# Optimization experiments

Measured on AMD Instinct MI355X. Metric: run time of the kernel, lower is better.

Reference implementation:

```python
import jax, jax.numpy as jnp
import numpy as np

EPS = 1e-10


def setup_inputs() -> dict:
    key = jax.random.key(0)
    k1, k2 = jax.random.split(key)
    x = jax.random.normal(k1, (64, 512, 256), dtype=jnp.float32)          # (N, code_dim, T)
    codebooks = jax.random.normal(k2, (6, 1024, 512), dtype=jnp.float32)  # (Q, nb_code, code_dim)
    return {"x": x, "codebooks": codebooks}


def _quantize_layer(x_flat, cb):
    # x_flat: (NT, D), cb: (C, D)
    dist = (jnp.sum(x_flat * x_flat, axis=-1, keepdims=True)
            - 2.0 * (x_flat @ cb.T)
            + jnp.sum(cb * cb, axis=-1))          # (NT, C)
    idx = jnp.argmin(dist, axis=-1)               # (NT,)
    x_d = cb[idx]                                 # gather, (NT, D)
    return idx, x_d


def reference(x, codebooks):
    N, D, T = x.shape
    Q, C, _ = codebooks.shape
    NT = N * T

    residual = x
    quantized_out = jnp.zeros_like(x)
    all_indices, losses, perps = [], [], []

    for q in range(Q):  # fixed small number of sequential quantizer stages
        cb = codebooks[q]
        # preprocess: (N, D, T) -> (NT, D)
        x_flat = residual.transpose(0, 2, 1).reshape(NT, D)
        idx, x_d = _quantize_layer(x_flat, cb)

        # commitment loss (codebook side detached; EMA-trained codebook)
        commit_loss = jnp.mean((x_flat - jax.lax.stop_gradient(x_d)) ** 2)

        # perplexity of code usage
        probs = jnp.zeros((C,), dtype=x.dtype).at[idx].add(1.0) / NT
        perplexity = jnp.exp(-jnp.sum(probs * jnp.log(probs + EPS)))

        # straight-through estimator, back to (N, D, T)
        quantized = x_flat + jax.lax.stop_gradient(x_d - x_flat)
        quantized = quantized.reshape(N, T, D).transpose(0, 2, 1)

        residual = residual - jax.lax.stop_gradient(quantized)
        quantized_out = quantized_out + quantized

        all_indices.append(idx.reshape(N, T))
        losses.append(commit_loss)
        perps.append(perplexity)

    all_indices = jnp.stack(all_indices, axis=-1)      # (N, T, Q)
    mean_loss = sum(losses) / Q
    mean_perplexity = sum(perps) / Q
    return quantized_out, all_indices, mean_loss, mean_perplexity
```

## Files before the change

### kernel.cpp

```cpp
#include <hip/hip_runtime.h>
#include <hip/hip_fp16.h>
#include <hip/hip_bf16.h>
#include <stdint.h>


#define NTROWS 16384
#define DDIM   512
#define CCODES 1024
#define QSTAGE 6

#define OFF_R      ((size_t)0)
#define OFF_RBF    ((size_t)33554432)
#define OFF_CBBF   ((size_t)50331648)
#define OFF_CAND   ((size_t)56623104)
#define OFF_CBSQ   ((size_t)58720256)
#define OFF_HIST   ((size_t)58744832)
#define OFF_LOSS   ((size_t)58769408)
#define WS_END     ((size_t)58775552)

#define OUT_IDX_OFF  ((size_t)8388608)
#define OUT_SCAL_OFF ((size_t)8486912)

typedef __attribute__((ext_vector_type(8))) short short8;
typedef __attribute__((ext_vector_type(8))) unsigned short ushort8v;
typedef __attribute__((ext_vector_type(4))) float f32x4;

__device__ __forceinline__ unsigned short f2bf(float f) {
    uint32_t u = __float_as_uint(f);
    uint32_t r = (u + 0x7fffu + ((u >> 16) & 1u)) >> 16;
    return (unsigned short)r;
}
__device__ __forceinline__ uint32_t fkey(float f) {
    uint32_t u = __float_as_uint(f);
    return u ^ ((uint32_t)((int32_t)u >> 31) | 0x80000000u);
}
__device__ __forceinline__ float funkey(uint32_t k) {
    uint32_t u = (k & 0x80000000u) ? (k ^ 0x80000000u) : ~k;
    return __uint_as_float(u);
}
__device__ __forceinline__ uint32_t umin32(uint32_t a, uint32_t b) { return a < b ? a : b; }
__device__ __forceinline__ uint32_t umax32(uint32_t a, uint32_t b) { return a > b ? a : b; }
__device__ __forceinline__ float wave_sum(float v) {
    for (int m = 32; m; m >>= 1) v += __shfl_xor(v, m, 64);
    return v;
}
__device__ __forceinline__ uint32_t wave_min_u32(uint32_t v) {
    for (int m = 32; m; m >>= 1) v = umin32(v, (uint32_t)__shfl_xor((int)v, m, 64));
    return v;
}
__device__ __forceinline__ void async_load16(const void* g, void* l) {
    __builtin_amdgcn_global_load_lds(
        (__attribute__((address_space(1))) void*)(void*)g,
        (__attribute__((address_space(3))) void*)l, 16, 0, 0);
}

__global__ __launch_bounds__(256) void prep_kernel(
    const float* __restrict__ x, const float* __restrict__ cb,
    float* __restrict__ r, unsigned short* __restrict__ rbf,
    unsigned short* __restrict__ cbbf, float* __restrict__ cbsq,
    unsigned int* __restrict__ hist, float* __restrict__ loss_bins)
{
    __shared__ float tile[32][33];
    if (blockIdx.x < 1536) {
        const int wave = threadIdx.x >> 6, lane = threadIdx.x & 63;
        const int row = blockIdx.x * 4 + wave;
        const float* p = cb + (size_t)row * DDIM;
        unsigned short* pb = cbbf + (size_t)row * DDIM;
        float s = 0.f;
#pragma unroll
        for (int t = 0; t < 8; ++t) {
            float v = p[lane + 64 * t];
            pb[lane + 64 * t] = f2bf(v);
            s += v * v;
        }
        s = wave_sum(s);
        if (lane == 0) cbsq[row] = s;
        if (blockIdx.x == 0) {
            for (int i = threadIdx.x; i < QSTAGE * CCODES; i += 256) hist[i] = 0u;
            for (int i = threadIdx.x; i < QSTAGE * 256; i += 256) loss_bins[i] = 0.f;
        }
    } else {
        const int bidx = blockIdx.x - 1536;
        const int d0 = (bidx & 15) * 32;
        const int t0 = ((bidx >> 4) & 7) * 32;
        const int n  = bidx >> 7;
        const int tx = threadIdx.x & 31, ty = threadIdx.x >> 5;
        const float* xp = x + (size_t)n * (DDIM * 256);
#pragma unroll
        for (int s = 0; s < 4; ++s) {
            int dd = ty + s * 8;
            tile[dd][tx] = xp[(size_t)(d0 + dd) * 256 + t0 + tx];
        }
        __syncthreads();
#pragma unroll
        for (int s = 0; s < 4; ++s) {
            int tt = ty + s * 8;
            float v = tile[tx][tt];
            size_t off = (size_t)(n * 256 + t0 + tt) * DDIM + d0 + tx;
            r[off] = v;
            rbf[off] = f2bf(v);
        }
    }
}

__global__ __launch_bounds__(256, 2) void gemm_dist_kernel(
    const unsigned short* __restrict__ Abf,
    const unsigned short* __restrict__ Bbf,
    const float* __restrict__ cbsq,
    uint32_t* __restrict__ cand)
{
    __shared__ __align__(16) unsigned short lA[128 * 32];
    __shared__ __align__(16) unsigned short lB[256 * 32];
    const int tid = threadIdx.x;
    const int wave = tid >> 6, lane = tid & 63;
    const int quad = lane >> 4, l15 = lane & 15;
    const int tm = blockIdx.x, tn2 = blockIdx.y;
    const int wm = wave & 1, wn = wave >> 1;

    f32x4 acc[4][8];
#pragma unroll
    for (int i = 0; i < 4; ++i)
#pragma unroll
        for (int j = 0; j < 8; ++j) acc[i][j] = (f32x4){0.f, 0.f, 0.f, 0.f};

    const int srow = wave * 16 + (lane >> 2);
    const int gchunk = (lane & 3) ^ ((lane >> 3) & 3);
    const unsigned short* gA0 = Abf + (size_t)(tm * 128 + srow) * DDIM + gchunk * 8;
    const unsigned short* gA1 = gA0 + 64 * DDIM;
    const unsigned short* gB0 = Bbf + (size_t)(tn2 * 256 + srow) * DDIM + gchunk * 8;
    const unsigned short* gB1 = gB0 + 64 * DDIM;
    const unsigned short* gB2 = gB0 + 128 * DDIM;
    const unsigned short* gB3 = gB0 + 192 * DDIM;
    unsigned short* sA0 = &lA[srow * 32 + (lane & 3) * 8];
    unsigned short* sA1 = &lA[(64 + srow) * 32 + (lane & 3) * 8];
    unsigned short* sB0 = &lB[srow * 32 + (lane & 3) * 8];
    unsigned short* sB1 = &lB[(64 + srow) * 32 + (lane & 3) * 8];
    unsigned short* sB2 = &lB[(128 + srow) * 32 + (lane & 3) * 8];
    unsigned short* sB3 = &lB[(192 + srow) * 32 + (lane & 3) * 8];

    for (int kt = 0; kt < DDIM / 32; ++kt) {
        async_load16(gA0, sA0); async_load16(gA1, sA1);
        async_load16(gB0, sB0); async_load16(gB1, sB1);
        async_load16(gB2, sB2); async_load16(gB3, sB3);
        gA0 += 32; gA1 += 32; gB0 += 32; gB1 += 32; gB2 += 32; gB3 += 32;
        __syncthreads();
        const int cqa = (quad ^ ((l15 >> 1) & 3)) * 8;
        short8 af[4], bfr[8];
#pragma unroll
        for (int i = 0; i < 4; ++i)
            af[i] = *(const short8*)&lA[(wm * 64 + i * 16 + l15) * 32 + cqa];
#pragma unroll
        for (int j = 0; j < 8; ++j)
            bfr[j] = *(const short8*)&lB[(wn * 128 + j * 16 + l15) * 32 + cqa];
#pragma unroll
        for (int i = 0; i < 4; ++i)
#pragma unroll
            for (int j = 0; j < 8; ++j)
                acc[i][j] = __builtin_amdgcn_mfma_f32_16x16x32_bf16(
                    af[i], bfr[j], acc[i][j], 0, 0, 0);
        __syncthreads();
    }

    const int rowbase = tm * 128 + wm * 64 + quad * 4;
    const int colbase = tn2 * 256 + wn * 128 + l15;
    const int gbase = tn2 * 4 + wn * 2;
    float cbs[8];
#pragma unroll
    for (int j = 0; j < 8; ++j) cbs[j] = cbsq[colbase + j * 16];
#pragma unroll
    for (int i = 0; i < 4; ++i) {
#pragma unroll
        for (int reg = 0; reg < 4; ++reg) {
            const int row = rowbase + i * 16 + reg;
#pragma unroll
            for (int jh = 0; jh < 2; ++jh) {
                uint32_t k[4];
#pragma unroll
                for (int jj = 0; jj < 4; ++jj) {
                    const int j = jh * 4 + jj;
                    float dv = cbs[j] - 2.0f * acc[i][j][reg];
                    k[jj] = (fkey(dv) & ~1023u) | (uint32_t)(colbase + j * 16);
                }
                uint32_t m01 = umin32(k[0], k[1]), M01 = umax32(k[0], k[1]);
                uint32_t m23 = umin32(k[2], k[3]), M23 = umax32(k[2], k[3]);
                uint32_t k1 = umin32(m01, m23);
                uint32_t k2 = umin32(umax32(m01, m23), umin32(M01, M23));
#pragma unroll
                for (int m = 1; m < 16; m <<= 1) {
                    uint32_t o1 = (uint32_t)__shfl_xor((int)k1, m, 64);
                    uint32_t o2 = (uint32_t)__shfl_xor((int)k2, m, 64);
                    uint32_t n1 = umin32(k1, o1);
                    uint32_t n2 = umin32(umax32(k1, o1), umin32(k2, o2));
                    k1 = n1; k2 = n2;
                }
                if (l15 == 0)
                    *(uint2*)&cand[((size_t)row * 16 + gbase + jh) * 2] =
                        make_uint2(k1, k2);
            }
        }
    }
}

#define MARGIN 8.0f
__global__ __launch_bounds__(256) void refine_kernel(
    float* __restrict__ r, unsigned short* __restrict__ rbf,
    const float* __restrict__ cbq, const float* __restrict__ cbsqq,
    const uint32_t* __restrict__ cand,
    float* __restrict__ out_idx, unsigned int* __restrict__ histq,
    float* __restrict__ loss_bins, int q, int write_bf)
{
    const int wave = threadIdx.x >> 6, lane = threadIdx.x & 63;
    const int nt = blockIdx.x * 4 + wave;

    const float4* r4 = (const float4*)(r + (size_t)nt * DDIM);
    float4 ra = r4[lane * 2], rb = r4[lane * 2 + 1];
    float s = ra.x * ra.x + ra.y * ra.y + ra.z * ra.z + ra.w * ra.w
            + rb.x * rb.x + rb.y * rb.y + rb.z * rb.z + rb.w * rb.w;
    const float sumx = wave_sum(s);

    uint32_t key = 0xFFFFFFFFu;
    if (lane < 32) key = cand[(size_t)nt * 32 + lane];
    const uint32_t kmin = wave_min_u32(key);
    const float thr = funkey(kmin & ~1023u) + MARGIN;

    unsigned long long mask = __ballot(lane < 32 && funkey(key & ~1023u) <= thr);

    float best = 1e30f;
    int bestc = CCODES;
    while (mask) {
        const int src = __ffsll(mask) - 1;
        mask &= mask - 1;
        const int cc = __shfl((int)(key & 1023u), src, 64);
        const float4* crow = (const float4*)(cbq + (size_t)cc * DDIM);
        float4 ca = crow[lane * 2], cb2 = crow[lane * 2 + 1];
        float dot = ra.x * ca.x + ra.y * ca.y + ra.z * ca.z + ra.w * ca.w
                  + rb.x * cb2.x + rb.y * cb2.y + rb.z * cb2.z + rb.w * cb2.w;
        dot = wave_sum(dot);
        const float de = (sumx - 2.0f * dot) + cbsqq[cc];
        if (de < best || (de == best && cc < bestc)) { best = de; bestc = cc; }
    }

    const float4* cbest = (const float4*)(cbq + (size_t)bestc * DDIM);
    float4 ba = cbest[lane * 2], bb = cbest[lane * 2 + 1];
    float4 na = make_float4(ra.x - ba.x, ra.y - ba.y, ra.z - ba.z, ra.w - ba.w);
    float4 nb = make_float4(rb.x - bb.x, rb.y - bb.y, rb.z - bb.z, rb.w - bb.w);
    float4* rw = (float4*)(r + (size_t)nt * DDIM);
    rw[lane * 2] = na; rw[lane * 2 + 1] = nb;
    if (write_bf) {
        ushort8v pk;
        pk[0] = f2bf(na.x); pk[1] = f2bf(na.y); pk[2] = f2bf(na.z); pk[3] = f2bf(na.w);
        pk[4] = f2bf(nb.x); pk[5] = f2bf(nb.y); pk[6] = f2bf(nb.z); pk[7] = f2bf(nb.w);
        *(ushort8v*)(rbf + (size_t)nt * DDIM + lane * 8) = pk;
    }

    if (lane == 0) {
        out_idx[(size_t)nt * QSTAGE + q] = (float)bestc;
        atomicAdd(&histq[bestc], 1u);
        atomicAdd(&loss_bins[q * 256 + (blockIdx.x & 255)], best);
    }
}

__global__ __launch_bounds__(256) void final_kernel(
    const float* __restrict__ x, const float* __restrict__ r,
    float* __restrict__ out,
    const unsigned int* __restrict__ hist, const float* __restrict__ loss_bins,
    float* __restrict__ out2)
{
    __shared__ float tile[32][33];
    __shared__ float red[4];
    __shared__ float perp_acc;
    const int tid = threadIdx.x, wave = tid >> 6, lane = tid & 63;

    if (blockIdx.x < 8192) {
        const int bidx = blockIdx.x;
        const int d0 = (bidx & 15) * 32;
        const int t0 = ((bidx >> 4) & 7) * 32;
        const int n  = bidx >> 7;
        const int tx = tid & 31, ty = tid >> 5;
#pragma unroll
        for (int s = 0; s < 4; ++s) {
            int tt = ty + s * 8;
            tile[tt][tx] = r[(size_t)(n * 256 + t0 + tt) * DDIM + d0 + tx];
        }
        __syncthreads();
        const float* xp = x + (size_t)n * (DDIM * 256);
        float* op = out + (size_t)n * (DDIM * 256);
#pragma unroll
        for (int s = 0; s < 4; ++s) {
            int dd = ty + s * 8;
            size_t off = (size_t)(d0 + dd) * 256 + t0 + tx;
            op[off] = xp[off] - tile[tx][dd];
        }
        return;
    }

    if (tid == 0) perp_acc = 0.f;
    __syncthreads();
    for (int q = 0; q < QSTAGE; ++q) {
        float s = 0.f;
        for (int c = tid; c < CCODES; c += 256) {
            float p = (float)hist[q * CCODES + c] * (1.0f / (float)NTROWS);
            s += p * logf(p + 1e-10f);
        }
        s = wave_sum(s);
        if (lane == 0) red[wave] = s;
        __syncthreads();
        if (tid == 0) {
            float tot = red[0] + red[1] + red[2] + red[3];
            perp_acc += expf(-tot);
        }
        __syncthreads();
    }
    float ls = 0.f;
    for (int i = tid; i < QSTAGE * 256; i += 256) ls += loss_bins[i];
    ls = wave_sum(ls);
    if (lane == 0) red[wave] = ls;
    __syncthreads();
    if (tid == 0) {
        float lsum = red[0] + red[1] + red[2] + red[3];
        out2[0] = (lsum / (float)QSTAGE) / ((float)NTROWS * (float)DDIM);
        out2[1] = perp_acc / (float)QSTAGE;
    }
}

extern "C" void kernel_launch(void* const* d_in, const int* in_sizes, int n_in,
                              void* d_out, int out_size, void* d_ws, size_t ws_size,
                              hipStream_t stream)
{
    const float* x  = (const float*)d_in[0];
    const float* cb = (const float*)d_in[1];
    float* out = (float*)d_out;
    char* ws = (char*)d_ws;

    float*          r      = (float*)(ws + OFF_R);
    unsigned short* rbf    = (unsigned short*)(ws + OFF_RBF);
    unsigned short* cbbf   = (unsigned short*)(ws + OFF_CBBF);
    uint32_t*       cand   = (uint32_t*)(ws + OFF_CAND);
    float*          cbsq   = (float*)(ws + OFF_CBSQ);
    unsigned int*   hist   = (unsigned int*)(ws + OFF_HIST);
    float*          lbins  = (float*)(ws + OFF_LOSS);

    prep_kernel<<<9728, 256, 0, stream>>>(x, cb, r, rbf, cbbf, cbsq, hist, lbins);

    for (int q = 0; q < QSTAGE; ++q) {
        const size_t cboff = (size_t)q * CCODES * DDIM;
        gemm_dist_kernel<<<dim3(128, 4), 256, 0, stream>>>(
            rbf, cbbf + cboff, cbsq + q * CCODES, cand);
        refine_kernel<<<4096, 256, 0, stream>>>(
            r, rbf, cb + cboff, cbsq + q * CCODES, cand,
            out + OUT_IDX_OFF, hist + q * CCODES, lbins,
            q, (q < QSTAGE - 1) ? 1 : 0);
    }

    final_kernel<<<8193, 256, 0, stream>>>(x, r, out, hist, lbins,
                                           out + OUT_SCAL_OFF);
}
```

Before: 476.0 us.

## Fuse previous-stage refine into next-stage distance GEMM with ping-pong buffers

Each stage's exact refine step now runs at the start of the next stage's bf16 distance GEMM kernel. Each block refines its own 128 rows and writes fp32 and bf16 residuals before loading them as the GEMM A operand. Residuals and candidate lists ping-pong between two buffers, one of which is the output buffer used as scratch. The final stage keeps a standalone refine kernel. This removes one launch per stage and a residual round trip, but the refine is repeated by all four column blocks for the same rows and runs serially, 32 rows per wave, with much less parallelism. The candidate margin also tightens from 8 to 2, and the A-operand loads get a cache-policy bit.

```diff
diff --git a/kernel.cpp b/kernel.cpp
--- a/kernel.cpp
+++ b/kernel.cpp
@@ -9,17 +9,20 @@
 #define CCODES 1024
 #define QSTAGE 6
 
-#define OFF_R      ((size_t)0)
+#define OFF_R0     ((size_t)0)
 #define OFF_RBF    ((size_t)33554432)
 #define OFF_CBBF   ((size_t)50331648)
-#define OFF_CAND   ((size_t)56623104)
-#define OFF_CBSQ   ((size_t)58720256)
-#define OFF_HIST   ((size_t)58744832)
-#define OFF_LOSS   ((size_t)58769408)
-#define WS_END     ((size_t)58775552)
+#define OFF_CAND0  ((size_t)56623104)
+#define OFF_CAND1  ((size_t)58720256)
+#define OFF_CBSQ   ((size_t)60817408)
+#define OFF_HIST   ((size_t)60841984)
+#define OFF_LOSS   ((size_t)60866560)
+#define WS_END     ((size_t)60872704)
 
 #define OUT_IDX_OFF  ((size_t)8388608)
 #define OUT_SCAL_OFF ((size_t)8486912)
+
+#define MARGIN 2.0f
 
 typedef __attribute__((ext_vector_type(8))) short short8;
 typedef __attribute__((ext_vector_type(8))) unsigned short ushort8v;
@@ -48,181 +51,26 @@
     for (int m = 32; m; m >>= 1) v = umin32(v, (uint32_t)__shfl_xor((int)v, m, 64));
     return v;
 }
+template <int AUX>
 __device__ __forceinline__ void async_load16(const void* g, void* l) {
     __builtin_amdgcn_global_load_lds(
         (__attribute__((address_space(1))) void*)(void*)g,
-        (__attribute__((address_space(3))) void*)l, 16, 0, 0);
-}
-
-__global__ __launch_bounds__(256) void prep_kernel(
-    const float* __restrict__ x, const float* __restrict__ cb,
-    float* __restrict__ r, unsigned short* __restrict__ rbf,
-    unsigned short* __restrict__ cbbf, float* __restrict__ cbsq,
-    unsigned int* __restrict__ hist, float* __restrict__ loss_bins)
-{
-    __shared__ float tile[32][33];
-    if (blockIdx.x < 1536) {
-        const int wave = threadIdx.x >> 6, lane = threadIdx.x & 63;
-        const int row = blockIdx.x * 4 + wave;
-        const float* p = cb + (size_t)row * DDIM;
-        unsigned short* pb = cbbf + (size_t)row * DDIM;
-        float s = 0.f;
-#pragma unroll
-        for (int t = 0; t < 8; ++t) {
-            float v = p[lane + 64 * t];
-            pb[lane + 64 * t] = f2bf(v);
-            s += v * v;
-        }
-        s = wave_sum(s);
-        if (lane == 0) cbsq[row] = s;
-        if (blockIdx.x == 0) {
-            for (int i = threadIdx.x; i < QSTAGE * CCODES; i += 256) hist[i] = 0u;
-            for (int i = threadIdx.x; i < QSTAGE * 256; i += 256) loss_bins[i] = 0.f;
-        }
-    } else {
-        const int bidx = blockIdx.x - 1536;
-        const int d0 = (bidx & 15) * 32;
-        const int t0 = ((bidx >> 4) & 7) * 32;
-        const int n  = bidx >> 7;
-        const int tx = threadIdx.x & 31, ty = threadIdx.x >> 5;
-        const float* xp = x + (size_t)n * (DDIM * 256);
-#pragma unroll
-        for (int s = 0; s < 4; ++s) {
-            int dd = ty + s * 8;
-            tile[dd][tx] = xp[(size_t)(d0 + dd) * 256 + t0 + tx];
-        }
-        __syncthreads();
-#pragma unroll
-        for (int s = 0; s < 4; ++s) {
-            int tt = ty + s * 8;
-            float v = tile[tx][tt];
-            size_t off = (size_t)(n * 256 + t0 + tt) * DDIM + d0 + tx;
-            r[off] = v;
-            rbf[off] = f2bf(v);
-        }
-    }
-}
-
-__global__ __launch_bounds__(256, 2) void gemm_dist_kernel(
-    const unsigned short* __restrict__ Abf,
-    const unsigned short* __restrict__ Bbf,
-    const float* __restrict__ cbsq,
-    uint32_t* __restrict__ cand)
-{
-    __shared__ __align__(16) unsigned short lA[128 * 32];
-    __shared__ __align__(16) unsigned short lB[256 * 32];
-    const int tid = threadIdx.x;
-    const int wave = tid >> 6, lane = tid & 63;
-    const int quad = lane >> 4, l15 = lane & 15;
-    const int tm = blockIdx.x, tn2 = blockIdx.y;
-    const int wm = wave & 1, wn = wave >> 1;
-
-    f32x4 acc[4][8];
-#pragma unroll
-    for (int i = 0; i < 4; ++i)
-#pragma unroll
-        for (int j = 0; j < 8; ++j) acc[i][j] = (f32x4){0.f, 0.f, 0.f, 0.f};
-
-    const int srow = wave * 16 + (lane >> 2);
-    const int gchunk = (lane & 3) ^ ((lane >> 3) & 3);
-    const unsigned short* gA0 = Abf + (size_t)(tm * 128 + srow) * DDIM + gchunk * 8;
-    const unsigned short* gA1 = gA0 + 64 * DDIM;
-    const unsigned short* gB0 = Bbf + (size_t)(tn2 * 256 + srow) * DDIM + gchunk * 8;
-    const unsigned short* gB1 = gB0 + 64 * DDIM;
-    const unsigned short* gB2 = gB0 + 128 * DDIM;
-    const unsigned short* gB3 = gB0 + 192 * DDIM;
-    unsigned short* sA0 = &lA[srow * 32 + (lane & 3) * 8];
-    unsigned short* sA1 = &lA[(64 + srow) * 32 + (lane & 3) * 8];
-    unsigned short* sB0 = &lB[srow * 32 + (lane & 3) * 8];
-    unsigned short* sB1 = &lB[(64 + srow) * 32 + (lane & 3) * 8];
-    unsigned short* sB2 = &lB[(128 + srow) * 32 + (lane & 3) * 8];
-    unsigned short* sB3 = &lB[(192 + srow) * 32 + (lane & 3) * 8];
-
-    for (int kt = 0; kt < DDIM / 32; ++kt) {
-        async_load16(gA0, sA0); async_load16(gA1, sA1);
-        async_load16(gB0, sB0); async_load16(gB1, sB1);
-        async_load16(gB2, sB2); async_load16(gB3, sB3);
-        gA0 += 32; gA1 += 32; gB0 += 32; gB1 += 32; gB2 += 32; gB3 += 32;
-        __syncthreads();
-        const int cqa = (quad ^ ((l15 >> 1) & 3)) * 8;
-        short8 af[4], bfr[8];
-#pragma unroll
-        for (int i = 0; i < 4; ++i)
-            af[i] = *(const short8*)&lA[(wm * 64 + i * 16 + l15) * 32 + cqa];
-#pragma unroll
-        for (int j = 0; j < 8; ++j)
-            bfr[j] = *(const short8*)&lB[(wn * 128 + j * 16 + l15) * 32 + cqa];
-#pragma unroll
-        for (int i = 0; i < 4; ++i)
-#pragma unroll
-            for (int j = 0; j < 8; ++j)
-                acc[i][j] = __builtin_amdgcn_mfma_f32_16x16x32_bf16(
-                    af[i], bfr[j], acc[i][j], 0, 0, 0);
-        __syncthreads();
-    }
-
-    const int rowbase = tm * 128 + wm * 64 + quad * 4;
-    const int colbase = tn2 * 256 + wn * 128 + l15;
-    const int gbase = tn2 * 4 + wn * 2;
-    float cbs[8];
-#pragma unroll
-    for (int j = 0; j < 8; ++j) cbs[j] = cbsq[colbase + j * 16];
-#pragma unroll
-    for (int i = 0; i < 4; ++i) {
-#pragma unroll
-        for (int reg = 0; reg < 4; ++reg) {
-            const int row = rowbase + i * 16 + reg;
-#pragma unroll
-            for (int jh = 0; jh < 2; ++jh) {
-                uint32_t k[4];
-#pragma unroll
-                for (int jj = 0; jj < 4; ++jj) {
-                    const int j = jh * 4 + jj;
-                    float dv = cbs[j] - 2.0f * acc[i][j][reg];
-                    k[jj] = (fkey(dv) & ~1023u) | (uint32_t)(colbase + j * 16);
-                }
-                uint32_t m01 = umin32(k[0], k[1]), M01 = umax32(k[0], k[1]);
-                uint32_t m23 = umin32(k[2], k[3]), M23 = umax32(k[2], k[3]);
-                uint32_t k1 = umin32(m01, m23);
-                uint32_t k2 = umin32(umax32(m01, m23), umin32(M01, M23));
-#pragma unroll
-                for (int m = 1; m < 16; m <<= 1) {
-                    uint32_t o1 = (uint32_t)__shfl_xor((int)k1, m, 64);
-                    uint32_t o2 = (uint32_t)__shfl_xor((int)k2, m, 64);
-                    uint32_t n1 = umin32(k1, o1);
-                    uint32_t n2 = umin32(umax32(k1, o1), umin32(k2, o2));
-                    k1 = n1; k2 = n2;
-                }
-                if (l15 == 0)
-                    *(uint2*)&cand[((size_t)row * 16 + gbase + jh) * 2] =
-                        make_uint2(k1, k2);
-            }
-        }
-    }
-}
-
-#define MARGIN 8.0f
-__global__ __launch_bounds__(256) void refine_kernel(
-    float* __restrict__ r, unsigned short* __restrict__ rbf,
-    const float* __restrict__ cbq, const float* __restrict__ cbsqq,
-    const uint32_t* __restrict__ cand,
-    float* __restrict__ out_idx, unsigned int* __restrict__ histq,
-    float* __restrict__ loss_bins, int q, int write_bf)
-{
-    const int wave = threadIdx.x >> 6, lane = threadIdx.x & 63;
-    const int nt = blockIdx.x * 4 + wave;
-
-    const float4* r4 = (const float4*)(r + (size_t)nt * DDIM);
-    float4 ra = r4[lane * 2], rb = r4[lane * 2 + 1];
+        (__attribute__((address_space(3))) void*)l, 16, 0, AUX);
+}
+
+__device__ __forceinline__ void refine_core(
+    int nt, int lane, float4 ra, float4 rb, uint32_t key,
+    float* r_out, unsigned short* rbf,
+    const float* cbq, const float* cbsqq,
+    float* out_idx, unsigned int* histq, float* loss_bins,
+    int q, int write_bf, int do_side)
+{
     float s = ra.x * ra.x + ra.y * ra.y + ra.z * ra.z + ra.w * ra.w
             + rb.x * rb.x + rb.y * rb.y + rb.z * rb.z + rb.w * rb.w;
     const float sumx = wave_sum(s);
 
-    uint32_t key = 0xFFFFFFFFu;
-    if (lane < 32) key = cand[(size_t)nt * 32 + lane];
     const uint32_t kmin = wave_min_u32(key);
     const float thr = funkey(kmin & ~1023u) + MARGIN;
-
     unsigned long long mask = __ballot(lane < 32 && funkey(key & ~1023u) <= thr);
 
     float best = 1e30f;
@@ -244,7 +92,7 @@
     float4 ba = cbest[lane * 2], bb = cbest[lane * 2 + 1];
     float4 na = make_float4(ra.x - ba.x, ra.y - ba.y, ra.z - ba.z, ra.w - ba.w);
     float4 nb = make_float4(rb.x - bb.x, rb.y - bb.y, rb.z - bb.z, rb.w - bb.w);
-    float4* rw = (float4*)(r + (size_t)nt * DDIM);
+    float4* rw = (float4*)(r_out + (size_t)nt * DDIM);
     rw[lane * 2] = na; rw[lane * 2 + 1] = nb;
     if (write_bf) {
         ushort8v pk;
@@ -252,12 +100,202 @@
         pk[4] = f2bf(nb.x); pk[5] = f2bf(nb.y); pk[6] = f2bf(nb.z); pk[7] = f2bf(nb.w);
         *(ushort8v*)(rbf + (size_t)nt * DDIM + lane * 8) = pk;
     }
-
-    if (lane == 0) {
+    if (do_side && lane == 0) {
         out_idx[(size_t)nt * QSTAGE + q] = (float)bestc;
         atomicAdd(&histq[bestc], 1u);
-        atomicAdd(&loss_bins[q * 256 + (blockIdx.x & 255)], best);
-    }
+        atomicAdd(&loss_bins[q * 256 + (nt & 255)], best);
+    }
+}
+
+__global__ __launch_bounds__(256) void prep_kernel(
+    const float* __restrict__ x, const float* __restrict__ cb,
+    float* __restrict__ r, unsigned short* __restrict__ rbf,
+    unsigned short* __restrict__ cbbf, float* __restrict__ cbsq,
+    unsigned int* __restrict__ hist, float* __restrict__ loss_bins)
+{
+    __shared__ float tile[32][33];
+    if (blockIdx.x < 1536) {
+        const int wave = threadIdx.x >> 6, lane = threadIdx.x & 63;
+        const int row = blockIdx.x * 4 + wave;
+        const float* p = cb + (size_t)row * DDIM;
+        unsigned short* pb = cbbf + (size_t)row * DDIM;
+        float s = 0.f;
+#pragma unroll
+        for (int t = 0; t < 8; ++t) {
+            float v = p[lane + 64 * t];
+            pb[lane + 64 * t] = f2bf(v);
+            s += v * v;
+        }
+        s = wave_sum(s);
+        if (lane == 0) cbsq[row] = s;
+        if (blockIdx.x == 0) {
+            for (int i = threadIdx.x; i < QSTAGE * CCODES; i += 256) hist[i] = 0u;
+            for (int i = threadIdx.x; i < QSTAGE * 256; i += 256) loss_bins[i] = 0.f;
+        }
+    } else {
+        const int bidx = blockIdx.x - 1536;
+        const int d0 = (bidx & 15) * 32;
+        const int t0 = ((bidx >> 4) & 7) * 32;
+        const int n  = bidx >> 7;
+        const int tx = threadIdx.x & 31, ty = threadIdx.x >> 5;
+        const float* xp = x + (size_t)n * (DDIM * 256);
+#pragma unroll
+        for (int s = 0; s < 4; ++s) {
+            int dd = ty + s * 8;
+            tile[dd][tx] = xp[(size_t)(d0 + dd) * 256 + t0 + tx];
+        }
+        __syncthreads();
+#pragma unroll
+        for (int s = 0; s < 4; ++s) {
+            int tt = ty + s * 8;
+            float v = tile[tx][tt];
+            size_t off = (size_t)(n * 256 + t0 + tt) * DDIM + d0 + tx;
+            r[off] = v;
+            rbf[off] = f2bf(v);
+        }
+    }
+}
+
+__global__ __launch_bounds__(256, 2) void fused_kernel(
+    const float* __restrict__ r_in, float* __restrict__ r_out,
+    unsigned short* rbf,
+    const unsigned short* __restrict__ Bbf,
+    const float* __restrict__ cbsq_g,
+    const uint32_t* __restrict__ cand_in,
+    uint32_t* __restrict__ cand_out,
+    const float* cb_prev, const float* cbsq_prev,
+    float* out_idx, unsigned int* hist_prev, float* loss_bins,
+    int q_prev, int do_refine)
+{
+    __shared__ __align__(16) unsigned short lA[128 * 32];
+    __shared__ __align__(16) unsigned short lB[256 * 32];
+    const int tid = threadIdx.x;
+    const int wave = tid >> 6, lane = tid & 63;
+    const int quad = lane >> 4, l15 = lane & 15;
+    const int tm = blockIdx.x, tn2 = blockIdx.y;
+    const int wm = wave & 1, wn = wave >> 1;
+
+    if (do_refine) {
+        const int do_side = (tn2 == 0);
+        int nt = tm * 128 + wave * 32;
+        const float4* r4 = (const float4*)(r_in + (size_t)nt * DDIM);
+        float4 ra = r4[lane * 2], rb = r4[lane * 2 + 1];
+        uint32_t key = (lane < 32) ? cand_in[(size_t)nt * 32 + lane] : 0xFFFFFFFFu;
+        for (int rr = 0; rr < 32; ++rr, ++nt) {
+            float4 pa = make_float4(0.f, 0.f, 0.f, 0.f), pb = pa;
+            uint32_t pkey = 0xFFFFFFFFu;
+            if (rr < 31) {
+                const float4* r4n = (const float4*)(r_in + (size_t)(nt + 1) * DDIM);
+                pa = r4n[lane * 2]; pb = r4n[lane * 2 + 1];
+                if (lane < 32) pkey = cand_in[(size_t)(nt + 1) * 32 + lane];
+            }
+            refine_core(nt, lane, ra, rb, key, r_out, rbf,
+                        cb_prev, cbsq_prev, out_idx, hist_prev, loss_bins,
+                        q_prev, 1, do_side);
+            ra = pa; rb = pb; key = pkey;
+        }
+        __threadfence_block();
+        __syncthreads();
+    }
+
+    f32x4 acc[4][8];
+#pragma unroll
+    for (int i = 0; i < 4; ++i)
+#pragma unroll
+        for (int j = 0; j < 8; ++j) acc[i][j] = (f32x4){0.f, 0.f, 0.f, 0.f};
+
+    const int srow = wave * 16 + (lane >> 2);
+    const int gchunk = (lane & 3) ^ ((lane >> 3) & 3);
+    const unsigned short* gA0 = rbf + (size_t)(tm * 128 + srow) * DDIM + gchunk * 8;
+    const unsigned short* gA1 = gA0 + 64 * DDIM;
+    const unsigned short* gB0 = Bbf + (size_t)(tn2 * 256 + srow) * DDIM + gchunk * 8;
+    const unsigned short* gB1 = gB0 + 64 * DDIM;
+    const unsigned short* gB2 = gB0 + 128 * DDIM;
+    const unsigned short* gB3 = gB0 + 192 * DDIM;
+    unsigned short* sA0 = &lA[srow * 32 + (lane & 3) * 8];
+    unsigned short* sA1 = &lA[(64 + srow) * 32 + (lane & 3) * 8];
+    unsigned short* sB0 = &lB[srow * 32 + (lane & 3) * 8];
+    unsigned short* sB1 = &lB[(64 + srow) * 32 + (lane & 3) * 8];
+    unsigned short* sB2 = &lB[(128 + srow) * 32 + (lane & 3) * 8];
+    unsigned short* sB3 = &lB[(192 + srow) * 32 + (lane & 3) * 8];
+
+    for (int kt = 0; kt < DDIM / 32; ++kt) {
+        async_load16<1>(gA0, sA0); async_load16<1>(gA1, sA1);
+        async_load16<0>(gB0, sB0); async_load16<0>(gB1, sB1);
+        async_load16<0>(gB2, sB2); async_load16<0>(gB3, sB3);
+        gA0 += 32; gA1 += 32; gB0 += 32; gB1 += 32; gB2 += 32; gB3 += 32;
+        __syncthreads();
+        const int cqa = (quad ^ ((l15 >> 1) & 3)) * 8;
+        short8 af[4], bfr[8];
+#pragma unroll
+        for (int i = 0; i < 4; ++i)
+            af[i] = *(const short8*)&lA[(wm * 64 + i * 16 + l15) * 32 + cqa];
+#pragma unroll
+        for (int j = 0; j < 8; ++j)
+            bfr[j] = *(const short8*)&lB[(wn * 128 + j * 16 + l15) * 32 + cqa];
+#pragma unroll
+        for (int i = 0; i < 4; ++i)
+#pragma unroll
+            for (int j = 0; j < 8; ++j)
+                acc[i][j] = __builtin_amdgcn_mfma_f32_16x16x32_bf16(
+                    af[i], bfr[j], acc[i][j], 0, 0, 0);
+        __syncthreads();
+    }
+
+    const int rowbase = tm * 128 + wm * 64 + quad * 4;
+    const int colbase = tn2 * 256 + wn * 128 + l15;
+    const int gbase = tn2 * 4 + wn * 2;
+    float cbs[8];
+#pragma unroll
+    for (int j = 0; j < 8; ++j) cbs[j] = cbsq_g[colbase + j * 16];
+#pragma unroll
+    for (int i = 0; i < 4; ++i) {
+#pragma unroll
+        for (int reg = 0; reg < 4; ++reg) {
+            const int row = rowbase + i * 16 + reg;
+#pragma unroll
+            for (int jh = 0; jh < 2; ++jh) {
+                uint32_t k[4];
+#pragma unroll
+                for (int jj = 0; jj < 4; ++jj) {
+                    const int j = jh * 4 + jj;
+                    float dv = cbs[j] - 2.0f * acc[i][j][reg];
+                    k[jj] = (fkey(dv) & ~1023u) | (uint32_t)(colbase + j * 16);
+                }
+                uint32_t m01 = umin32(k[0], k[1]), M01 = umax32(k[0], k[1]);
+                uint32_t m23 = umin32(k[2], k[3]), M23 = umax32(k[2], k[3]);
+                uint32_t k1 = umin32(m01, m23);
+                uint32_t k2 = umin32(umax32(m01, m23), umin32(M01, M23));
+#pragma unroll
+                for (int m = 1; m < 16; m <<= 1) {
+                    uint32_t o1 = (uint32_t)__shfl_xor((int)k1, m, 64);
+                    uint32_t o2 = (uint32_t)__shfl_xor((int)k2, m, 64);
+                    uint32_t n1 = umin32(k1, o1);
+                    uint32_t n2 = umin32(umax32(k1, o1), umin32(k2, o2));
+                    k1 = n1; k2 = n2;
+                }
+                if (l15 == 0)
+                    *(uint2*)&cand_out[((size_t)row * 16 + gbase + jh) * 2] =
+                        make_uint2(k1, k2);
+            }
+        }
+    }
+}
+
+__global__ __launch_bounds__(256) void refine_kernel(
+    const float* __restrict__ r_in, float* __restrict__ r_out,
+    const float* __restrict__ cbq, const float* __restrict__ cbsqq,
+    const uint32_t* __restrict__ cand_in,
+    float* __restrict__ out_idx, unsigned int* __restrict__ histq,
+    float* __restrict__ loss_bins, int q)
+{
+    const int wave = threadIdx.x >> 6, lane = threadIdx.x & 63;
+    const int nt = blockIdx.x * 4 + wave;
+    const float4* r4 = (const float4*)(r_in + (size_t)nt * DDIM);
+    float4 ra = r4[lane * 2], rb = r4[lane * 2 + 1];
+    uint32_t key = (lane < 32) ? cand_in[(size_t)nt * 32 + lane] : 0xFFFFFFFFu;
+    refine_core(nt, lane, ra, rb, key, r_out, (unsigned short*)0,
+                cbq, cbsqq, out_idx, histq, loss_bins, q, 0, 1);
 }
 
 __global__ __launch_bounds__(256) void final_kernel(
@@ -332,26 +370,39 @@
     float* out = (float*)d_out;
     char* ws = (char*)d_ws;
 
-    float*          r      = (float*)(ws + OFF_R);
+    float*          r_even = (float*)(ws + OFF_R0);
+    float*          r_odd  = out;
     unsigned short* rbf    = (unsigned short*)(ws + OFF_RBF);
     unsigned short* cbbf   = (unsigned short*)(ws + OFF_CBBF);
-    uint32_t*       cand   = (uint32_t*)(ws + OFF_CAND);
+    uint32_t*       cand0  = (uint32_t*)(ws + OFF_CAND0);
+    uint32_t*       cand1  = (uint32_t*)(ws + OFF_CAND1);
     float*          cbsq   = (float*)(ws + OFF_CBSQ);
     unsigned int*   hist   = (unsigned int*)(ws + OFF_HIST);
     float*          lbins  = (float*)(ws + OFF_LOSS);
 
-    prep_kernel<<<9728, 256, 0, stream>>>(x, cb, r, rbf, cbbf, cbsq, hist, lbins);
+    prep_kernel<<<9728, 256, 0, stream>>>(x, cb, r_even, rbf, cbbf, cbsq,
+                                          hist, lbins);
 
     for (int q = 0; q < QSTAGE; ++q) {
-        const size_t cboff = (size_t)q * CCODES * DDIM;
-        gemm_dist_kernel<<<dim3(128, 4), 256, 0, stream>>>(
-            rbf, cbbf + cboff, cbsq + q * CCODES, cand);
-        refine_kernel<<<4096, 256, 0, stream>>>(
-            r, rbf, cb + cboff, cbsq + q * CCODES, cand,
-            out + OUT_IDX_OFF, hist + q * CCODES, lbins,
-            q, (q < QSTAGE - 1) ? 1 : 0);
-    }
-
-    final_kernel<<<8193, 256, 0, stream>>>(x, r, out, hist, lbins,
+        const size_t cbo  = (size_t)q * CCODES * DDIM;
+        const int    qp   = (q > 0) ? (q - 1) : 0;
+        const size_t cbop = (size_t)qp * CCODES * DDIM;
+        const float* rin  = (qp % 2 == 0) ? r_even : r_odd;
+        float*       rout = (q  % 2 == 0) ? r_even : r_odd;
+        const uint32_t* cin  = (qp % 2 == 0) ? cand0 : cand1;
+        uint32_t*       cout = (q  % 2 == 0) ? cand0 : cand1;
+        fused_kernel<<<dim3(128, 4), 256, 0, stream>>>(
+            rin, rout, rbf, cbbf + cbo, cbsq + q * CCODES,
+            cin, cout,
+            cb + cbop, cbsq + qp * CCODES,
+            out + OUT_IDX_OFF, hist + qp * CCODES, lbins,
+            qp, (q > 0) ? 1 : 0);
+    }
+
+    refine_kernel<<<4096, 256, 0, stream>>>(
+        r_odd, r_even, cb + (size_t)5 * CCODES * DDIM, cbsq + 5 * CCODES,
+        cand1, out + OUT_IDX_OFF, hist + 5 * CCODES, lbins, 5);
+
+    final_kernel<<<8193, 256, 0, stream>>>(x, r_even, out, hist, lbins,
                                            out + OUT_SCAL_OFF);
 }
```

After: 569.9 us. 19.7% more time.
